# Performance work log

Hardware: AMD Instinct MI355X
Metric: run time of the kernel (lower is better)

The kernel has to match this reference:

```python
import jax, jax.numpy as jnp
import numpy as np

BS = 64   # sparsity_block_size
B, R, C = 8, 64, 64


def setup_inputs() -> dict:
    key = jax.random.key(0)
    # causal block-lower-triangular layout: block (r,c) present iff c <= r
    tril = jnp.tril(jnp.ones((R, C), dtype=jnp.int32))
    sparsity_layout = jnp.broadcast_to(tril[None], (B, R, C)).astype(jnp.int32)
    n_sparse_blocks = B * (R * (R + 1) // 2)  # 16640
    x = jax.random.normal(key, (n_sparse_blocks, BS, BS), dtype=jnp.float32)
    return {"x": x, "sparsity_layout": sparsity_layout}


def reference(x, sparsity_layout):
    # x: [n_blocks, bs, bs]; sparsity_layout: [B, R, C] with sum == n_blocks.
    n, bs, _ = x.shape
    Bb, Rr, Cc = sparsity_layout.shape
    flat = sparsity_layout.reshape(-1)                       # [B*R*C]
    # reverse LUT: index into x for each present block (row-major nonzero order)
    rev = jnp.cumsum(flat) - 1                               # [B*R*C]
    present = (flat == 1)
    # to_dense (block form), fill -inf for absent blocks
    gathered = x[jnp.clip(rev, 0)]                           # [B*R*C, bs, bs]
    neg_inf = jnp.asarray(-jnp.inf, dtype=x.dtype)
    blocks = jnp.where(present[:, None, None], gathered, neg_inf)
    # arrange into dense rows: [B, R, bs, C*bs] (softmax over full dense last dim)
    rows = blocks.reshape(Bb, Rr, Cc, bs, bs).transpose(0, 1, 3, 2, 4).reshape(Bb, Rr, bs, Cc * bs)
    sm = jax.nn.softmax(rows, axis=-1)
    # back to block form
    sm_blocks = sm.reshape(Bb, Rr, bs, Cc, bs).transpose(0, 1, 3, 2, 4).reshape(Bb * Rr * Cc, bs, bs)
    # to_sparse: scatter present blocks back to their slots (absent -> dump slot n)
    idx = jnp.where(present, rev, n)
    out = jnp.zeros((n + 1, bs, bs), dtype=x.dtype).at[idx].set(sm_blocks)
    return out[:n]
```

## Files before the change

kernel.cpp:

```cpp
#include <hip/hip_runtime.h>
#include <math.h>


__global__ __launch_bounds__(256) void bs_softmax_kernel(
    const float* __restrict__ x, float* __restrict__ out) {
    const int bid = blockIdx.x;
    const int i   = bid & 63;
    const int r   = 63 - ((bid >> 6) & 63);
    const int b   = bid >> 12;

    const int base = (b * 2080 + ((r * (r + 1)) >> 1)) * 4096 + i * 64;
    const int nvec = (r + 1) << 4;

    const int t = threadIdx.x;

    float4 v[4];
    float m = -INFINITY;

    #pragma unroll
    for (int k = 0; k < 4; ++k) {
        const int vi = t + (k << 8);
        if (vi < nvec) {
            const int col = vi << 2;
            const int cb  = col >> 6;
            const int j   = col & 63;
            const float4 val = *(const float4*)(x + base + cb * 4096 + j);
            v[k] = val;
            m = fmaxf(m, fmaxf(fmaxf(val.x, val.y), fmaxf(val.z, val.w)));
        } else {
            v[k] = make_float4(-INFINITY, -INFINITY, -INFINITY, -INFINITY);
        }
    }

    #pragma unroll
    for (int off = 32; off >= 1; off >>= 1)
        m = fmaxf(m, __shfl_xor(m, off, 64));
    __shared__ float sm[4];
    __shared__ float ss[4];
    const int wave = t >> 6;
    if ((t & 63) == 0) sm[wave] = m;
    __syncthreads();
    m = fmaxf(fmaxf(sm[0], sm[1]), fmaxf(sm[2], sm[3]));

    float s = 0.0f;
    #pragma unroll
    for (int k = 0; k < 4; ++k) {
        float4 val = v[k];
        val.x = __expf(val.x - m);
        val.y = __expf(val.y - m);
        val.z = __expf(val.z - m);
        val.w = __expf(val.w - m);
        v[k] = val;
        s += (val.x + val.y) + (val.z + val.w);
    }
    #pragma unroll
    for (int off = 32; off >= 1; off >>= 1)
        s += __shfl_xor(s, off, 64);
    if ((t & 63) == 0) ss[wave] = s;
    __syncthreads();
    s = (ss[0] + ss[1]) + (ss[2] + ss[3]);
    const float inv = 1.0f / s;

    #pragma unroll
    for (int k = 0; k < 4; ++k) {
        const int vi = t + (k << 8);
        if (vi < nvec) {
            const int col = vi << 2;
            const int cb  = col >> 6;
            const int j   = col & 63;
            float4 val = v[k];
            val.x *= inv; val.y *= inv; val.z *= inv; val.w *= inv;
            *(float4*)(out + base + cb * 4096 + j) = val;
        }
    }
}

extern "C" void kernel_launch(void* const* d_in, const int* in_sizes, int n_in,
                              void* d_out, int out_size, void* d_ws, size_t ws_size,
                              hipStream_t stream) {
    const float* x = (const float*)d_in[0];
    float* out = (float*)d_out;
    dim3 grid(8 * 64 * 64);
    dim3 block(256);
    bs_softmax_kernel<<<grid, block, 0, stream>>>(x, out);
}
```

Baseline: 440.2 us.

## Assign one wavefront per softmax row instead of one block per row

Each 64-lane wavefront now handles a whole dense row, holding up to 16 float4 values per lane, and the block processes four rows. Max and sum reductions become pure wave shuffles, so the shared-memory exchange and both __syncthreads calls are gone. The grid shrinks by a factor of four, which removes most of the per-block launch overhead and the idle threads on short rows. The cost is higher register pressure from the 16-entry array and uneven row lengths within a block, since the four rows share the same r.

```diff
diff --git a/kernel.cpp b/kernel.cpp
--- a/kernel.cpp
+++ b/kernel.cpp
@@ -4,27 +4,28 @@
 
 __global__ __launch_bounds__(256) void bs_softmax_kernel(
     const float* __restrict__ x, float* __restrict__ out) {
-    const int bid = blockIdx.x;
-    const int i   = bid & 63;
-    const int r   = 63 - ((bid >> 6) & 63);
-    const int b   = bid >> 12;
+    const int w    = (blockIdx.x << 2) + (threadIdx.x >> 6);
+    const int lane = threadIdx.x & 63;
+
+    const int i = w & 63;
+    const int r = 63 - ((w >> 6) & 63);
+    const int b = w >> 12;
 
     const int base = (b * 2080 + ((r * (r + 1)) >> 1)) * 4096 + i * 64;
     const int nvec = (r + 1) << 4;
 
-    const int t = threadIdx.x;
+    const int j   = (lane << 2) & 63;
+    const int cb0 = lane >> 4;
+    const float* p0 = x + base + cb0 * 4096 + j;
 
-    float4 v[4];
+    float4 v[16];
     float m = -INFINITY;
 
     #pragma unroll
-    for (int k = 0; k < 4; ++k) {
-        const int vi = t + (k << 8);
+    for (int k = 0; k < 16; ++k) {
+        const int vi = lane + (k << 6);
         if (vi < nvec) {
-            const int col = vi << 2;
-            const int cb  = col >> 6;
-            const int j   = col & 63;
-            const float4 val = *(const float4*)(x + base + cb * 4096 + j);
+            const float4 val = *(const float4*)(p0 + k * 16384);
             v[k] = val;
             m = fmaxf(m, fmaxf(fmaxf(val.x, val.y), fmaxf(val.z, val.w)));
         } else {
@@ -35,16 +36,10 @@
     #pragma unroll
     for (int off = 32; off >= 1; off >>= 1)
         m = fmaxf(m, __shfl_xor(m, off, 64));
-    __shared__ float sm[4];
-    __shared__ float ss[4];
-    const int wave = t >> 6;
-    if ((t & 63) == 0) sm[wave] = m;
-    __syncthreads();
-    m = fmaxf(fmaxf(sm[0], sm[1]), fmaxf(sm[2], sm[3]));
 
     float s = 0.0f;
     #pragma unroll
-    for (int k = 0; k < 4; ++k) {
+    for (int k = 0; k < 16; ++k) {
         float4 val = v[k];
         val.x = __expf(val.x - m);
         val.y = __expf(val.y - m);
@@ -56,21 +51,16 @@
     #pragma unroll
     for (int off = 32; off >= 1; off >>= 1)
         s += __shfl_xor(s, off, 64);
-    if ((t & 63) == 0) ss[wave] = s;
-    __syncthreads();
-    s = (ss[0] + ss[1]) + (ss[2] + ss[3]);
     const float inv = 1.0f / s;
 
+    float* q0 = out + base + cb0 * 4096 + j;
     #pragma unroll
-    for (int k = 0; k < 4; ++k) {
-        const int vi = t + (k << 8);
+    for (int k = 0; k < 16; ++k) {
+        const int vi = lane + (k << 6);
         if (vi < nvec) {
-            const int col = vi << 2;
-            const int cb  = col >> 6;
-            const int j   = col & 63;
             float4 val = v[k];
             val.x *= inv; val.y *= inv; val.z *= inv; val.w *= inv;
-            *(float4*)(out + base + cb * 4096 + j) = val;
+            *(float4*)(q0 + k * 16384) = val;
         }
     }
 }
@@ -80,7 +70,7 @@
                               hipStream_t stream) {
     const float* x = (const float*)d_in[0];
     float* out = (float*)d_out;
-    dim3 grid(8 * 64 * 64);
+    dim3 grid(8 * 64 * 64 / 4);
     dim3 block(256);
     bs_softmax_kernel<<<grid, block, 0, stream>>>(x, out);
 }
```

Result: no change. 436.4 us (-0.8%).
